# Optimization experiments

Measured on AMD Instinct MI355X. Metric: run time of the kernel, lower is better.

## Reference

```python
import jax, jax.numpy as jnp
import numpy as np

N = 38332        # nodes = poi_len - 1 (pinned by fc_layer in_features)
POI_LEN = 38333
CAT_LEN = 400
POI_DIM = 300
CAT_DIM = 100
C = 128          # gcn_channel
L = 5            # gcn_layers
E = 1200000      # edges
NEG = 0.01       # nn.LeakyReLU default slope
GAT_NEG = 0.2    # GATConv attention slope


def _leaky(x, s=NEG):
    return jnp.where(x > 0, x, s * x)


def _gcn_conv(x, W, b, src, dst, ew):
    # PyG GCNConv: self-loops already appended in (src,dst,ew); symmetric norm
    xw = x @ W
    deg = jax.ops.segment_sum(ew, dst, num_segments=N)
    dinv = jnp.where(deg > 0, jax.lax.rsqrt(deg), 0.0)
    norm = dinv[src] * ew * dinv[dst]
    out = jax.ops.segment_sum(xw[src] * norm[:, None], dst, num_segments=N)
    return out + b


def _gat_conv(x, W, a_src, a_dst, b, src, dst):
    # PyG GATConv, 1 head; self-loops already in (src,dst)
    xw = x @ W                      # [N, C]
    al = xw @ a_src                 # [N]
    ar = xw @ a_dst                 # [N]
    e = _leaky(al[src] + ar[dst], GAT_NEG)          # [E+N]
    emax = jax.ops.segment_max(e, dst, num_segments=N)
    ex = jnp.exp(e - emax[dst])
    denom = jax.ops.segment_sum(ex, dst, num_segments=N)
    att = ex / denom[dst]
    out = jax.ops.segment_sum(xw[src] * att[:, None], dst, num_segments=N)
    return out + b


def _graph_norm(x, gamma, beta, alpha, eps=1e-5):
    # PyG GraphNorm over the single graph (all nodes)
    mean = x.mean(0)
    xc = x - alpha * mean
    var = (xc * xc).mean(0)
    return gamma * xc * jax.lax.rsqrt(var + eps) + beta


def _forward(poi_ids, cat_ids, feat3, edge_index, edge_weight, poi_emb, cat_emb,
             Win, b_in, gcn_W, gcn_b, gn_gamma, gn_beta, gn_alpha,
             gat_W, gat_asrc, gat_adst, gat_b, Wout, b_out,
             fc_W1, fc_b1, fc_W2, fc_b2):
    loops = jnp.arange(N, dtype=edge_index.dtype)
    src = jnp.concatenate([edge_index[0], loops])
    dst = jnp.concatenate([edge_index[1], loops])
    ew = jnp.concatenate([edge_weight, jnp.ones((N,), edge_weight.dtype)])
    # node features: [poi_emb | cat_emb | 3 raw floats] -> [N, 403]
    feat = jnp.concatenate([poi_emb[poi_ids], cat_emb[cat_ids], feat3], axis=1)
    x = _leaky(_gcn_conv(feat, Win, b_in, src, dst, ew))
    for l in range(L):  # GcnUnit stack (shared GraphNorm within a unit)
        t = _leaky(_graph_norm(_gcn_conv(x, gcn_W[l], gcn_b[l], src, dst, ew),
                               gn_gamma[l], gn_beta[l], gn_alpha[l]))
        x = x + t
        t = _leaky(_graph_norm(_gat_conv(x, gat_W[l], gat_asrc[l], gat_adst[l], gat_b[l], src, dst),
                               gn_gamma[l], gn_beta[l], gn_alpha[l]))
        x = x + t
    x = _leaky(_gcn_conv(x, Wout, b_out, src, dst, ew)).reshape(-1)  # [N]
    h = jax.nn.relu(x @ fc_W1 + fc_b1)
    return jax.nn.relu(h @ fc_W2 + fc_b2)  # [POI_LEN]


def setup_inputs() -> dict:
    key = jax.random.key(0)
    ks = iter(jax.random.split(key, 24))
    nrm = lambda s, sc=0.05: jax.random.normal(next(ks), s, dtype=jnp.float32) * sc
    return {
        'poi_ids': jax.random.randint(next(ks), (N,), 0, POI_LEN),
        'cat_ids': jax.random.randint(next(ks), (N,), 0, CAT_LEN),
        'feat3': jax.random.normal(next(ks), (N, 3), dtype=jnp.float32),
        'edge_index': jax.random.randint(next(ks), (2, E), 0, N),
        'edge_weight': jax.random.uniform(next(ks), (E,), dtype=jnp.float32),
        'poi_emb': nrm((POI_LEN, POI_DIM)),
        'cat_emb': nrm((CAT_LEN, CAT_DIM)),
        'Win': nrm((POI_DIM + CAT_DIM + 3, C)),
        'b_in': jnp.zeros((C,), jnp.float32),
        'gcn_W': nrm((L, C, C)),
        'gcn_b': jnp.zeros((L, C), jnp.float32),
        'gn_gamma': jnp.ones((L, C), jnp.float32),
        'gn_beta': jnp.zeros((L, C), jnp.float32),
        'gn_alpha': jnp.ones((L, C), jnp.float32),
        'gat_W': nrm((L, C, C)),
        'gat_asrc': nrm((L, C)),
        'gat_adst': nrm((L, C)),
        'gat_b': jnp.zeros((L, C), jnp.float32),
        'Wout': nrm((C, 1)),
        'b_out': jnp.zeros((1,), jnp.float32),
        'fc_W1': nrm((N, 128)),
        'fc_b1': jnp.zeros((128,), jnp.float32),
        'fc_W2': nrm((128, POI_LEN)),
        'fc_b2': jnp.zeros((POI_LEN,), jnp.float32),
    }


def reference(poi_ids, cat_ids, feat3, edge_index, edge_weight, poi_emb, cat_emb,
              Win, b_in, gcn_W, gcn_b, gn_gamma, gn_beta, gn_alpha,
              gat_W, gat_asrc, gat_adst, gat_b, Wout, b_out,
              fc_W1, fc_b1, fc_W2, fc_b2):
    return _forward(poi_ids, cat_ids, feat3, edge_index, edge_weight, poi_emb, cat_emb,
                    Win, b_in, gcn_W, gcn_b, gn_gamma, gn_beta, gn_alpha,
                    gat_W, gat_asrc, gat_adst, gat_b, Wout, b_out,
                    fc_W1, fc_b1, fc_W2, fc_b2)
```

## Files before the change

kernel.cpp:

```cpp
#include <hip/hip_runtime.h>

typedef unsigned short ushort_t;
typedef __attribute__((ext_vector_type(8))) short short8v;
typedef __attribute__((ext_vector_type(4))) float floatx4;

__device__ __forceinline__ float b2f(ushort_t u) {
    unsigned int x = ((unsigned int)u) << 16;
    float f; __builtin_memcpy(&f, &x, 4); return f;
}
__device__ __forceinline__ ushort_t f2b(float f) {
    unsigned int x; __builtin_memcpy(&x, &f, 4);
    unsigned int lsb = (x >> 16) & 1u;
    x += 0x7fffu + lsb;
    return (ushort_t)(x >> 16);
}
__device__ __forceinline__ float leaky01(float v) { return v > 0.f ? v : 0.01f * v; }

__global__ void init_k(int* cnt, int N) {
    int i = blockIdx.x * 256 + threadIdx.x;
    if (i < N) cnt[i] = 1;
}

__global__ void count_k(const int* __restrict__ ei, int* cnt, int* pos, int E) {
    int e = blockIdx.x * 256 + threadIdx.x;
    if (e < E) pos[e] = atomicAdd(&cnt[ei[E + e]], 1);
}

__launch_bounds__(1024)
__global__ void scan_k(const int* __restrict__ cnt, int* rp, int n) {
    __shared__ int wsum[16];
    int tid = threadIdx.x; int lane = tid & 63, wid = tid >> 6;
    int base = 0;
    for (int start = 0; start < n; start += 4096) {
        int v[4]; int s = 0;
        #pragma unroll
        for (int j = 0; j < 4; ++j) {
            int i = start + tid * 4 + j;
            v[j] = (i < n) ? cnt[i] : 0; s += v[j];
        }
        int sc = s;
        #pragma unroll
        for (int off = 1; off < 64; off <<= 1) {
            int t = __shfl_up(sc, off);
            if (lane >= off) sc += t;
        }
        if (lane == 63) wsum[wid] = sc;
        __syncthreads();
        if (wid == 0) {
            int ws = (lane < 16) ? wsum[lane] : 0;
            #pragma unroll
            for (int off = 1; off < 16; off <<= 1) {
                int t = __shfl_up(ws, off);
                if (lane >= off) ws += t;
            }
            if (lane < 16) wsum[lane] = ws;
        }
        __syncthreads();
        int wbase = (wid > 0) ? wsum[wid - 1] : 0;
        int excl = base + wbase + (sc - s);
        #pragma unroll
        for (int j = 0; j < 4; ++j) {
            int i = start + tid * 4 + j;
            if (i < n) rp[i] = excl;
            excl += v[j];
        }
        int total = wsum[15];
        __syncthreads();
        base += total;
    }
    if (tid == 0) rp[n] = base;
}

__global__ void post_k(const int* __restrict__ rp, float2* er, int N) {
    int i = blockIdx.x * 256 + threadIdx.x;
    if (i < N) er[rp[i]] = make_float2(__int_as_float(i), 1.0f);
}

__global__ void scat_k(const int* __restrict__ ei, const float* __restrict__ ew,
                       const int* __restrict__ rp, const int* __restrict__ pos,
                       float2* er, int E) {
    int e = blockIdx.x * 256 + threadIdx.x;
    if (e < E) {
        int dst = ei[E + e];
        er[rp[dst] + pos[e]] = make_float2(__int_as_float(ei[e]), ew[e]);
    }
}

__global__ void deg_k(const int* __restrict__ rp, const float2* __restrict__ er,
                      float* dinv, int N) {
    int wave = threadIdx.x >> 6, lane = threadIdx.x & 63;
    int node = blockIdx.x * 4 + wave;
    if (node >= N) return;
    int s0 = rp[node], end = rp[node + 1];
    float sum = 0.f;
    for (int s = s0 + lane; s < end; s += 64) sum += er[s].y;
    #pragma unroll
    for (int off = 32; off; off >>= 1) sum += __shfl_xor(sum, off);
    if (lane == 0) dinv[node] = rsqrtf(sum);
}

__global__ void prep_w(const float* __restrict__ gcn_W, const float* __restrict__ gat_W,
                       const float* __restrict__ Win, ushort_t* __restrict__ wt,
                       ushort_t* __restrict__ wtin) {
    int idx = blockIdx.x * 256 + threadIdx.x;
    if (idx < 10 * 16384) {
        int l = idx >> 14, r = idx & 16383;
        int n = r >> 7, k = r & 127;
        const float* src = (l < 5) ? (gcn_W + l * 16384) : (gat_W + (l - 5) * 16384);
        wt[idx] = f2b(src[k * 128 + n]);
    } else {
        int idx2 = idx - 10 * 16384;
        if (idx2 < 128 * 320) {
            int n = idx2 / 320, k = idx2 - n * 320;
            wtin[idx2] = f2b(k < 300 ? Win[k * 128 + n] : 0.f);
        }
    }
}

__global__ void cat_proj_k(const float* __restrict__ ce, const float* __restrict__ Win,
                           float* __restrict__ cp) {
    __shared__ float row[100];
    int r = blockIdx.x, tid = threadIdx.x;
    if (tid < 100) row[tid] = ce[r * 100 + tid];
    __syncthreads();
    float acc = 0.f;
    #pragma unroll 4
    for (int k = 0; k < 100; ++k) acc += row[k] * Win[(300 + k) * 128 + tid];
    cp[r * 128 + tid] = acc;
}

__launch_bounds__(256)
__global__ void poi_gemm(const float* __restrict__ pe, const ushort_t* __restrict__ wtin,
                         ushort_t* __restrict__ pp, int P) {
    __shared__ __align__(16) ushort_t As[64 * 328];
    int tid = threadIdx.x;
    int wid = tid >> 6, lane = tid & 63;
    int r0 = blockIdx.x * 64;
    #pragma unroll
    for (int p = 0; p < 80; ++p) {
        int idx = tid + p * 256;
        int row = idx / 320, k = idx - row * 320;
        float v = 0.f;
        if (k < 300 && (r0 + row) < P) v = pe[(size_t)(r0 + row) * 300 + k];
        As[row * 328 + k] = f2b(v);
    }
    __syncthreads();
    int m = lane & 15, q = lane >> 4;
    short8v af[10];
    #pragma unroll
    for (int kc = 0; kc < 10; ++kc)
        af[kc] = *(const short8v*)&As[(wid * 16 + m) * 328 + kc * 32 + q * 8];
    #pragma unroll
    for (int ct = 0; ct < 8; ++ct) {
        const ushort_t* wr = wtin + (size_t)(ct * 16 + m) * 320 + q * 8;
        floatx4 acc = {0.f, 0.f, 0.f, 0.f};
        #pragma unroll
        for (int kc = 0; kc < 10; ++kc) {
            short8v b = *(const short8v*)(wr + kc * 32);
            acc = __builtin_amdgcn_mfma_f32_16x16x32_bf16(af[kc], b, acc, 0, 0, 0);
        }
        int col = ct * 16 + m;
        #pragma unroll
        for (int rg = 0; rg < 4; ++rg) {
            int row = r0 + wid * 16 + q * 4 + rg;
            if (row < P) pp[(size_t)row * 128 + col] = f2b(acc[rg]);
        }
    }
}

template <int NORM, int ALAR>
__launch_bounds__(256)
__global__ void gemm_fused(float* __restrict__ x, const float* __restrict__ gsrc,
                           const float* __restrict__ mom,
                           const float* __restrict__ gamma, const float* __restrict__ beta,
                           const float* __restrict__ alpha,
                           const ushort_t* __restrict__ wt,
                           const float* __restrict__ asrc, const float* __restrict__ adst,
                           ushort_t* __restrict__ xw,
                           float* __restrict__ al, float* __restrict__ ar, int N) {
    __shared__ __align__(16) ushort_t As[64 * 136];
    __shared__ float sc[128], sh[128];
    int tid = threadIdx.x;
    if (NORM) {
        if (tid < 128) {
            float mmean = mom[tid] / (float)N;
            float a = alpha[tid];
            float var = mom[128 + tid] / (float)N - 2.f * a * mmean * mmean + a * a * mmean * mmean;
            float s = gamma[tid] * rsqrtf(var + 1e-5f);
            sc[tid] = s;
            sh[tid] = beta[tid] - s * a * mmean;
        }
        __syncthreads();
    }
    int r0 = blockIdx.x * 64;
    #pragma unroll
    for (int p = 0; p < 8; ++p) {
        int idx = tid + p * 256;
        int row = idx >> 5, c4 = (idx & 31) * 4;
        int grow = r0 + row;
        float4 xv = make_float4(0.f, 0.f, 0.f, 0.f);
        if (grow < N) {
            xv = *(const float4*)&x[(size_t)grow * 128 + c4];
            if (NORM) {
                float4 gv = *(const float4*)&gsrc[(size_t)grow * 128 + c4];
                xv.x += leaky01(sc[c4] * gv.x + sh[c4]);
                xv.y += leaky01(sc[c4 + 1] * gv.y + sh[c4 + 1]);
                xv.z += leaky01(sc[c4 + 2] * gv.z + sh[c4 + 2]);
                xv.w += leaky01(sc[c4 + 3] * gv.w + sh[c4 + 3]);
                *(float4*)&x[(size_t)grow * 128 + c4] = xv;
            }
        }
        ushort4 b;
        b.x = f2b(xv.x); b.y = f2b(xv.y); b.z = f2b(xv.z); b.w = f2b(xv.w);
        *(ushort4*)&As[row * 136 + c4] = b;
    }
    __syncthreads();
    int wid = tid >> 6, lane = tid & 63;
    int m = lane & 15, q = lane >> 4;
    const int arr = (wid * 16 + m) * 136 + q * 8;
    short8v a0 = *(const short8v*)&As[arr];
    short8v a1 = *(const short8v*)&As[arr + 32];
    short8v a2 = *(const short8v*)&As[arr + 64];
    short8v a3 = *(const short8v*)&As[arr + 96];
    float alsum[4] = {0.f, 0.f, 0.f, 0.f}, arsum[4] = {0.f, 0.f, 0.f, 0.f};
    #pragma unroll
    for (int ct = 0; ct < 8; ++ct) {
        const ushort_t* wr = wt + (size_t)(ct * 16 + m) * 128 + q * 8;
        short8v b0 = *(const short8v*)(wr);
        short8v b1 = *(const short8v*)(wr + 32);
        short8v b2 = *(const short8v*)(wr + 64);
        short8v b3 = *(const short8v*)(wr + 96);
        floatx4 acc = {0.f, 0.f, 0.f, 0.f};
        acc = __builtin_amdgcn_mfma_f32_16x16x32_bf16(a0, b0, acc, 0, 0, 0);
        acc = __builtin_amdgcn_mfma_f32_16x16x32_bf16(a1, b1, acc, 0, 0, 0);
        acc = __builtin_amdgcn_mfma_f32_16x16x32_bf16(a2, b2, acc, 0, 0, 0);
        acc = __builtin_amdgcn_mfma_f32_16x16x32_bf16(a3, b3, acc, 0, 0, 0);
        int col = ct * 16 + m;
        if (ALAR) {
            float av = asrc[col], dv = adst[col];
            #pragma unroll
            for (int rg = 0; rg < 4; ++rg) {
                alsum[rg] += acc[rg] * av;
                arsum[rg] += acc[rg] * dv;
            }
        }
        #pragma unroll
        for (int rg = 0; rg < 4; ++rg) {
            int row = r0 + wid * 16 + q * 4 + rg;
            if (row < N) xw[(size_t)row * 128 + col] = f2b(acc[rg]);
        }
    }
    if (ALAR) {
        #pragma unroll
        for (int rg = 0; rg < 4; ++rg) {
            #pragma unroll
            for (int off = 1; off < 16; off <<= 1) {
                alsum[rg] += __shfl_xor(alsum[rg], off);
                arsum[rg] += __shfl_xor(arsum[rg], off);
            }
        }
        if (m == 0) {
            #pragma unroll
            for (int rg = 0; rg < 4; ++rg) {
                int row = r0 + wid * 16 + q * 4 + rg;
                if (row < N) { al[row] = alsum[rg]; ar[row] = arsum[rg]; }
            }
        }
    }
}

__global__ void combine_k(const ushort_t* __restrict__ pp, const float* __restrict__ cp,
                          const int* __restrict__ poi_ids, const int* __restrict__ cat_ids,
                          const float* __restrict__ feat3, const float* __restrict__ Win,
                          ushort_t* __restrict__ xw, int N) {
    __shared__ float wf0[128], wf1[128], wf2[128];
    int tid = threadIdx.x;
    if (tid < 128) {
        wf0[tid] = Win[400 * 128 + tid];
        wf1[tid] = Win[401 * 128 + tid];
        wf2[tid] = Win[402 * 128 + tid];
    }
    __syncthreads();
    int node = blockIdx.x * 2 + (tid >> 7);
    int c = tid & 127;
    if (node >= N) return;
    int pid = poi_ids[node], cid = cat_ids[node];
    float f0 = feat3[node * 3], f1 = feat3[node * 3 + 1], f2 = feat3[node * 3 + 2];
    float v = b2f(pp[(size_t)pid * 128 + c]) + cp[cid * 128 + c]
            + f0 * wf0[c] + f1 * wf1[c] + f2 * wf2[c];
    xw[(size_t)node * 128 + c] = f2b(v);
}

template <int MODE>
__launch_bounds__(256)
__global__ void agg_k(const ushort_t* __restrict__ xw, const int* __restrict__ rp,
                      const float2* __restrict__ er, const float* __restrict__ dinv,
                      const float* __restrict__ al, const float* __restrict__ ar,
                      const float* __restrict__ bias, float* __restrict__ g, int N) {
    int wave = threadIdx.x >> 6, lane = threadIdx.x & 63;
    int node = blockIdx.x * 4 + wave;
    if (node >= N) return;
    int s0 = __builtin_amdgcn_readfirstlane(rp[node]);
    int end = __builtin_amdgcn_readfirstlane(rp[node + 1]);
    int g8 = lane >> 4;
    int c8 = (lane & 15) * 8;
    float dn = 0.f, mmax = 0.f, inv = 0.f, ari = 0.f;
    if (MODE == 2) {
        ari = ar[node];
        float mm = -1e30f;
        for (int s = s0 + lane; s < end; s += 64) {
            int src = __float_as_int(er[s].x);
            float e = al[src] + ari; e = e > 0.f ? e : 0.2f * e;
            mm = fmaxf(mm, e);
        }
        #pragma unroll
        for (int off = 32; off; off >>= 1) mm = fmaxf(mm, __shfl_xor(mm, off));
        float ds = 0.f;
        for (int s = s0 + lane; s < end; s += 64) {
            int src = __float_as_int(er[s].x);
            float e = al[src] + ari; e = e > 0.f ? e : 0.2f * e;
            ds += __expf(e - mm);
        }
        #pragma unroll
        for (int off = 32; off; off >>= 1) ds += __shfl_xor(ds, off);
        mmax = mm;
        inv = 1.f / ds;
    } else {
        dn = dinv[node];
    }
    float acc[8] = {0.f, 0.f, 0.f, 0.f, 0.f, 0.f, 0.f, 0.f};
    auto body = [&](int e) {
        float2 r = er[e];
        int src = __float_as_int(r.x);
        float cf;
        if (MODE == 2) {
            float ev = al[src] + ari; ev = ev > 0.f ? ev : 0.2f * ev;
            cf = __expf(ev - mmax) * inv;
        } else {
            cf = dinv[src] * r.y * dn;
        }
        const short8v u = *(const short8v*)&xw[(size_t)src * 128 + c8];
        #pragma unroll
        for (int k = 0; k < 8; ++k) acc[k] += cf * b2f((ushort_t)u[k]);
    };
    int e = s0 + g8;
    for (; e + 12 < end; e += 16) { body(e); body(e + 4); body(e + 8); body(e + 12); }
    for (; e < end; e += 4) body(e);
    #pragma unroll
    for (int k = 0; k < 8; ++k) {
        acc[k] += __shfl_xor(acc[k], 16);
        acc[k] += __shfl_xor(acc[k], 32);
    }
    if (g8 == 0) {
        float4 o1, o2;
        o1.x = acc[0] + bias[c8];     o1.y = acc[1] + bias[c8 + 1];
        o1.z = acc[2] + bias[c8 + 2]; o1.w = acc[3] + bias[c8 + 3];
        o2.x = acc[4] + bias[c8 + 4]; o2.y = acc[5] + bias[c8 + 5];
        o2.z = acc[6] + bias[c8 + 6]; o2.w = acc[7] + bias[c8 + 7];
        if (MODE == 1) {
            o1.x = leaky01(o1.x); o1.y = leaky01(o1.y); o1.z = leaky01(o1.z); o1.w = leaky01(o1.w);
            o2.x = leaky01(o2.x); o2.y = leaky01(o2.y); o2.z = leaky01(o2.z); o2.w = leaky01(o2.w);
        }
        *(float4*)&g[(size_t)node * 128 + c8] = o1;
        *(float4*)&g[(size_t)node * 128 + c8 + 4] = o2;
    }
}

__global__ void moments_k(const float* __restrict__ g, float* mom, int n32) {
    __shared__ float s1s[256][4], s2s[256][4];
    int tid = threadIdx.x;
    long long T = (long long)gridDim.x * 256;
    float a1[4] = {0.f, 0.f, 0.f, 0.f}, a2[4] = {0.f, 0.f, 0.f, 0.f};
    const float4* g4 = (const float4*)g;
    for (long long idx = (long long)blockIdx.x * 256 + tid; idx < n32; idx += T) {
        float4 v = g4[idx];
        a1[0] += v.x; a2[0] += v.x * v.x;
        a1[1] += v.y; a2[1] += v.y * v.y;
        a1[2] += v.z; a2[2] += v.z * v.z;
        a1[3] += v.w; a2[3] += v.w * v.w;
    }
    #pragma unroll
    for (int j = 0; j < 4; ++j) { s1s[tid][j] = a1[j]; s2s[tid][j] = a2[j]; }
    __syncthreads();
    if (tid < 32) {
        float r1[4] = {0.f, 0.f, 0.f, 0.f}, r2[4] = {0.f, 0.f, 0.f, 0.f};
        for (int t = tid; t < 256; t += 32) {
            #pragma unroll
            for (int j = 0; j < 4; ++j) { r1[j] += s1s[t][j]; r2[j] += s2s[t][j]; }
        }
        #pragma unroll
        for (int j = 0; j < 4; ++j) {
            atomicAdd(&mom[4 * tid + j], r1[j]);
            atomicAdd(&mom[128 + 4 * tid + j], r2[j]);
        }
    }
}

__global__ void norm_ydot_k(const float* __restrict__ x, const float* __restrict__ g,
                            const float* __restrict__ mom,
                            const float* __restrict__ gamma, const float* __restrict__ beta,
                            const float* __restrict__ alpha, const float* __restrict__ Wout,
                            float* __restrict__ yv, int N) {
    __shared__ float sc[128], sh[128], wv[128];
    int tid = threadIdx.x;
    if (tid < 128) {
        float m = mom[tid] / (float)N;
        float a = alpha[tid];
        float var = mom[128 + tid] / (float)N - 2.f * a * m * m + a * a * m * m;
        float s = gamma[tid] * rsqrtf(var + 1e-5f);
        sc[tid] = s;
        sh[tid] = beta[tid] - s * a * m;
        wv[tid] = Wout[tid];
    }
    __syncthreads();
    int wave = tid >> 6, lane = tid & 63;
    int node = blockIdx.x * 4 + wave;
    if (node >= N) return;
    int c = lane * 2;
    float2 gv = *(const float2*)&g[(size_t)node * 128 + c];
    float2 xv = *(const float2*)&x[(size_t)node * 128 + c];
    float v0 = xv.x + leaky01(sc[c] * gv.x + sh[c]);
    float v1 = xv.y + leaky01(sc[c + 1] * gv.y + sh[c + 1]);
    float acc = v0 * wv[c] + v1 * wv[c + 1];
    #pragma unroll
    for (int off = 32; off; off >>= 1) acc += __shfl_xor(acc, off);
    if (lane == 0) yv[node] = acc;
}

__global__ void aggs_k(const float* __restrict__ yv, const int* __restrict__ rp,
                       const float2* __restrict__ er, const float* __restrict__ dinv,
                       const float* __restrict__ b_out, float* xs, int N) {
    int wave = threadIdx.x >> 6, lane = threadIdx.x & 63;
    int node = blockIdx.x * 4 + wave;
    if (node >= N) return;
    int s0 = rp[node], end = rp[node + 1];
    float dn = dinv[node];
    float acc = 0.f;
    for (int s = s0 + lane; s < end; s += 64) {
        float2 r = er[s];
        int src = __float_as_int(r.x);
        acc += dinv[src] * r.y * dn * yv[src];
    }
    #pragma unroll
    for (int off = 32; off; off >>= 1) acc += __shfl_xor(acc, off);
    if (lane == 0) xs[node] = leaky01(acc + b_out[0]);
}

__global__ void fc1_k(const float* __restrict__ xs, const float* __restrict__ W1,
                      float* hacc, int N) {
    __shared__ float sd[256];
    int tid = threadIdx.x;
    int j = tid & 127, half = tid >> 7;
    int r0 = blockIdx.x * 256;
    float acc = 0.f;
    for (int rr = half; rr < 256; rr += 2) {
        int r = r0 + rr;
        if (r < N) acc += xs[r] * W1[(size_t)r * 128 + j];
    }
    sd[tid] = acc;
    __syncthreads();
    if (tid < 128) atomicAdd(&hacc[tid], sd[tid] + sd[tid + 128]);
}

__global__ void fc2_k(const float* __restrict__ hacc, const float* __restrict__ b1,
                      const float* __restrict__ W2, const float* __restrict__ b2v,
                      float* out, int P) {
    __shared__ float hs[128];
    int tid = threadIdx.x;
    if (tid < 128) {
        float h = hacc[tid] + b1[tid];
        hs[tid] = h > 0.f ? h : 0.f;
    }
    __syncthreads();
    int p = blockIdx.x * 256 + tid;
    if (p >= P) return;
    float acc = 0.f;
    #pragma unroll 8
    for (int j = 0; j < 128; ++j) acc += hs[j] * W2[(size_t)j * P + p];
    acc += b2v[p];
    out[p] = acc > 0.f ? acc : 0.f;
}

extern "C" void kernel_launch(void* const* d_in, const int* in_sizes, int n_in,
                              void* d_out, int out_size, void* d_ws, size_t ws_size,
                              hipStream_t stream) {
    const int*   poi_ids  = (const int*)d_in[0];
    const int*   cat_ids  = (const int*)d_in[1];
    const float* feat3    = (const float*)d_in[2];
    const int*   ei       = (const int*)d_in[3];
    const float* ew       = (const float*)d_in[4];
    const float* poi_emb  = (const float*)d_in[5];
    const float* cat_emb  = (const float*)d_in[6];
    const float* Win      = (const float*)d_in[7];
    const float* b_in     = (const float*)d_in[8];
    const float* gcn_W    = (const float*)d_in[9];
    const float* gcn_b    = (const float*)d_in[10];
    const float* gn_gamma = (const float*)d_in[11];
    const float* gn_beta  = (const float*)d_in[12];
    const float* gn_alpha = (const float*)d_in[13];
    const float* gat_W    = (const float*)d_in[14];
    const float* gat_asrc = (const float*)d_in[15];
    const float* gat_adst = (const float*)d_in[16];
    const float* gat_b    = (const float*)d_in[17];
    const float* Wout     = (const float*)d_in[18];
    const float* b_out    = (const float*)d_in[19];
    const float* fc_W1    = (const float*)d_in[20];
    const float* fc_b1    = (const float*)d_in[21];
    const float* fc_W2    = (const float*)d_in[22];
    const float* fc_b2    = (const float*)d_in[23];

    const int N = in_sizes[0];
    const int E = in_sizes[4];
    const int POI = in_sizes[5] / 300;
    const int P = out_size;
    const int TOT = E + N;
    const int n128 = N * 128;
    const int n32 = n128 / 4;
    const int NPAD = ((N + 63) / 64) * 64;
    const int PPAD = ((POI + 63) / 64) * 64;

    char* w = (char*)d_ws;
    size_t off = 0;
    auto take = [&](size_t bytes) -> char* {
        char* p = w + off;
        off = (off + bytes + 255) & ~(size_t)255;
        return p;
    };
    float*    x    = (float*)take((size_t)n128 * 4);
    float*    g    = (float*)take((size_t)n128 * 4);
    ushort_t* xw   = (ushort_t*)take((size_t)NPAD * 128 * 2);
    ushort_t* pp   = (ushort_t*)take((size_t)PPAD * 128 * 2);
    float*    cp   = (float*)take((size_t)400 * 128 * 4);
    ushort_t* wt   = (ushort_t*)take((size_t)10 * 16384 * 2);
    ushort_t* wtin = (ushort_t*)take((size_t)128 * 320 * 2);
    int*    rp   = (int*)take((size_t)(N + 1) * 4);
    int*    cnt  = (int*)take((size_t)N * 4);
    int*    pos  = (int*)take((size_t)E * 4);
    float*  dinv = (float*)take((size_t)N * 4);
    float2* er   = (float2*)take((size_t)TOT * 8);
    float*  al   = (float*)take((size_t)N * 4);
    float*  ar   = (float*)take((size_t)N * 4);
    float*  yv   = (float*)take((size_t)N * 4);
    float*  xs   = (float*)take((size_t)N * 4);
    float*  mom  = (float*)take((size_t)(10 * 256 + 128) * 4);
    float*  hacc = mom + 10 * 256;

    const int gN   = (N + 255) / 256;
    const int gE   = (E + 255) / 256;
    const int gMM  = NPAD / 64;
    const int gPOI = PPAD / 64;
    const int gW   = (N + 3) / 4;
    const int gP   = (P + 255) / 256;

    hipMemsetAsync(mom, 0, (size_t)(10 * 256 + 128) * 4, stream);

    init_k<<<gN, 256, 0, stream>>>(cnt, N);
    count_k<<<gE, 256, 0, stream>>>(ei, cnt, pos, E);
    scan_k<<<1, 1024, 0, stream>>>(cnt, rp, N);
    post_k<<<gN, 256, 0, stream>>>(rp, er, N);
    scat_k<<<gE, 256, 0, stream>>>(ei, ew, rp, pos, er, E);
    deg_k<<<gW, 256, 0, stream>>>(rp, er, dinv, N);

    prep_w<<<(10 * 16384 + 128 * 320 + 255) / 256, 256, 0, stream>>>(gcn_W, gat_W, Win, wt, wtin);
    cat_proj_k<<<400, 128, 0, stream>>>(cat_emb, Win, cp);
    poi_gemm<<<gPOI, 256, 0, stream>>>(poi_emb, wtin, pp, POI);
    combine_k<<<(N + 1) / 2, 256, 0, stream>>>(pp, cp, poi_ids, cat_ids, feat3, Win, xw, N);
    agg_k<1><<<gW, 256, 0, stream>>>(xw, rp, er, dinv, nullptr, nullptr, b_in, x, N);

    for (int l = 0; l < 5; ++l) {
        if (l == 0)
            gemm_fused<0, 0><<<gMM, 256, 0, stream>>>(x, nullptr, nullptr, nullptr, nullptr,
                                                      nullptr, wt, nullptr, nullptr,
                                                      xw, nullptr, nullptr, N);
        else
            gemm_fused<1, 0><<<gMM, 256, 0, stream>>>(x, g, mom + (2 * l - 1) * 256,
                                                      gn_gamma + (l - 1) * 128,
                                                      gn_beta + (l - 1) * 128,
                                                      gn_alpha + (l - 1) * 128,
                                                      wt + (size_t)l * 16384, nullptr, nullptr,
                                                      xw, nullptr, nullptr, N);
        agg_k<0><<<gW, 256, 0, stream>>>(xw, rp, er, dinv, nullptr, nullptr,
                                         gcn_b + l * 128, g, N);
        moments_k<<<240, 256, 0, stream>>>(g, mom + (2 * l) * 256, n32);

        gemm_fused<1, 1><<<gMM, 256, 0, stream>>>(x, g, mom + (2 * l) * 256,
                                                  gn_gamma + l * 128, gn_beta + l * 128,
                                                  gn_alpha + l * 128,
                                                  wt + (size_t)(5 + l) * 16384,
                                                  gat_asrc + l * 128, gat_adst + l * 128,
                                                  xw, al, ar, N);
        agg_k<2><<<gW, 256, 0, stream>>>(xw, rp, er, nullptr, al, ar, gat_b + l * 128, g, N);
        moments_k<<<240, 256, 0, stream>>>(g, mom + (2 * l + 1) * 256, n32);
    }

    norm_ydot_k<<<gW, 256, 0, stream>>>(x, g, mom + 9 * 256, gn_gamma + 4 * 128,
                                        gn_beta + 4 * 128, gn_alpha + 4 * 128, Wout, yv, N);
    aggs_k<<<gW, 256, 0, stream>>>(yv, rp, er, dinv, b_out, xs, N);

    fc1_k<<<(N + 255) / 256, 256, 0, stream>>>(xs, fc_W1, hacc, N);
    fc2_k<<<gP, 256, 0, stream>>>(hacc, fc_b1, fc_W2, fc_b2, (float*)d_out, P);
}
```

Before: 1.454 ms.

## Precompute GCN edge coefficients, vectorize poi_gemm loads, deepen aggregation unroll

Adds a one-time pass that folds the symmetric normalization dinv[src]*w*dinv[dst] into the CSR edge array, so the GCN aggregation kernels and the final scalar aggregation read a ready coefficient instead of gathering dinv per edge. The poi_gemm staging loop now loads float4 rows and zero-fills the K padding separately. The aggregation inner loop is unrolled to 8 edges per group for more memory-level parallelism. It costs one extra kernel pass over the edges and more registers in agg_k.

```diff
diff --git a/kernel.cpp b/kernel.cpp
--- a/kernel.cpp
+++ b/kernel.cpp
@@ -97,6 +97,21 @@
     #pragma unroll
     for (int off = 32; off; off >>= 1) sum += __shfl_xor(sum, off);
     if (lane == 0) dinv[node] = rsqrtf(sum);
+}
+
+__global__ void coef_k(const int* __restrict__ rp, float2* er,
+                       const float* __restrict__ dinv, int N) {
+    int wave = threadIdx.x >> 6, lane = threadIdx.x & 63;
+    int node = blockIdx.x * 4 + wave;
+    if (node >= N) return;
+    int s0 = rp[node], end = rp[node + 1];
+    float dn = dinv[node];
+    for (int s = s0 + lane; s < end; s += 64) {
+        float2 r = er[s];
+        int src = __float_as_int(r.x);
+        r.y = dinv[src] * r.y * dn;
+        er[s] = r;
+    }
 }
 
 __global__ void prep_w(const float* __restrict__ gcn_W, const float* __restrict__ gat_W,
@@ -137,12 +152,25 @@
     int wid = tid >> 6, lane = tid & 63;
     int r0 = blockIdx.x * 64;
     #pragma unroll
-    for (int p = 0; p < 80; ++p) {
+    for (int p = 0; p < 19; ++p) {
         int idx = tid + p * 256;
-        int row = idx / 320, k = idx - row * 320;
-        float v = 0.f;
-        if (k < 300 && (r0 + row) < P) v = pe[(size_t)(r0 + row) * 300 + k];
-        As[row * 328 + k] = f2b(v);
+        if (idx < 4800) {
+            int row = idx / 75, kq = idx - row * 75;
+            int grow = r0 + row;
+            float4 v = make_float4(0.f, 0.f, 0.f, 0.f);
+            if (grow < P) v = *(const float4*)&pe[(size_t)grow * 300 + kq * 4];
+            ushort4 b;
+            b.x = f2b(v.x); b.y = f2b(v.y); b.z = f2b(v.z); b.w = f2b(v.w);
+            *(ushort4*)&As[row * 328 + kq * 4] = b;
+        }
+    }
+    #pragma unroll
+    for (int p = 0; p < 5; ++p) {
+        int idx = tid + p * 256;
+        if (idx < 1280) {
+            int row = idx / 20, j = idx - row * 20;
+            As[row * 328 + 300 + j] = 0;
+        }
     }
     __syncthreads();
     int m = lane & 15, q = lane >> 4;
@@ -294,7 +322,7 @@
 template <int MODE>
 __launch_bounds__(256)
 __global__ void agg_k(const ushort_t* __restrict__ xw, const int* __restrict__ rp,
-                      const float2* __restrict__ er, const float* __restrict__ dinv,
+                      const float2* __restrict__ er,
                       const float* __restrict__ al, const float* __restrict__ ar,
                       const float* __restrict__ bias, float* __restrict__ g, int N) {
     int wave = threadIdx.x >> 6, lane = threadIdx.x & 63;
@@ -304,7 +332,7 @@
     int end = __builtin_amdgcn_readfirstlane(rp[node + 1]);
     int g8 = lane >> 4;
     int c8 = (lane & 15) * 8;
-    float dn = 0.f, mmax = 0.f, inv = 0.f, ari = 0.f;
+    float mmax = 0.f, inv = 0.f, ari = 0.f;
     if (MODE == 2) {
         ari = ar[node];
         float mm = -1e30f;
@@ -325,8 +353,6 @@
         for (int off = 32; off; off >>= 1) ds += __shfl_xor(ds, off);
         mmax = mm;
         inv = 1.f / ds;
-    } else {
-        dn = dinv[node];
     }
     float acc[8] = {0.f, 0.f, 0.f, 0.f, 0.f, 0.f, 0.f, 0.f};
     auto body = [&](int e) {
@@ -337,14 +363,17 @@
             float ev = al[src] + ari; ev = ev > 0.f ? ev : 0.2f * ev;
             cf = __expf(ev - mmax) * inv;
         } else {
-            cf = dinv[src] * r.y * dn;
+            cf = r.y;
         }
         const short8v u = *(const short8v*)&xw[(size_t)src * 128 + c8];
         #pragma unroll
         for (int k = 0; k < 8; ++k) acc[k] += cf * b2f((ushort_t)u[k]);
     };
     int e = s0 + g8;
-    for (; e + 12 < end; e += 16) { body(e); body(e + 4); body(e + 8); body(e + 12); }
+    for (; e + 28 < end; e += 32) {
+        body(e);      body(e + 4);  body(e + 8);  body(e + 12);
+        body(e + 16); body(e + 20); body(e + 24); body(e + 28);
+    }
     for (; e < end; e += 4) body(e);
     #pragma unroll
     for (int k = 0; k < 8; ++k) {
@@ -428,18 +457,16 @@
 }
 
 __global__ void aggs_k(const float* __restrict__ yv, const int* __restrict__ rp,
-                       const float2* __restrict__ er, const float* __restrict__ dinv,
+                       const float2* __restrict__ er,
                        const float* __restrict__ b_out, float* xs, int N) {
     int wave = threadIdx.x >> 6, lane = threadIdx.x & 63;
     int node = blockIdx.x * 4 + wave;
     if (node >= N) return;
     int s0 = rp[node], end = rp[node + 1];
-    float dn = dinv[node];
     float acc = 0.f;
     for (int s = s0 + lane; s < end; s += 64) {
         float2 r = er[s];
-        int src = __float_as_int(r.x);
-        acc += dinv[src] * r.y * dn * yv[src];
+        acc += r.y * yv[__float_as_int(r.x)];
     }
     #pragma unroll
     for (int off = 32; off; off >>= 1) acc += __shfl_xor(acc, off);
@@ -560,12 +587,13 @@
     post_k<<<gN, 256, 0, stream>>>(rp, er, N);
     scat_k<<<gE, 256, 0, stream>>>(ei, ew, rp, pos, er, E);
     deg_k<<<gW, 256, 0, stream>>>(rp, er, dinv, N);
+    coef_k<<<gW, 256, 0, stream>>>(rp, er, dinv, N);
 
     prep_w<<<(10 * 16384 + 128 * 320 + 255) / 256, 256, 0, stream>>>(gcn_W, gat_W, Win, wt, wtin);
     cat_proj_k<<<400, 128, 0, stream>>>(cat_emb, Win, cp);
     poi_gemm<<<gPOI, 256, 0, stream>>>(poi_emb, wtin, pp, POI);
     combine_k<<<(N + 1) / 2, 256, 0, stream>>>(pp, cp, poi_ids, cat_ids, feat3, Win, xw, N);
-    agg_k<1><<<gW, 256, 0, stream>>>(xw, rp, er, dinv, nullptr, nullptr, b_in, x, N);
+    agg_k<1><<<gW, 256, 0, stream>>>(xw, rp, er, nullptr, nullptr, b_in, x, N);
 
     for (int l = 0; l < 5; ++l) {
         if (l == 0)
@@ -579,8 +607,7 @@
                                                       gn_alpha + (l - 1) * 128,
                                                       wt + (size_t)l * 16384, nullptr, nullptr,
                                                       xw, nullptr, nullptr, N);
-        agg_k<0><<<gW, 256, 0, stream>>>(xw, rp, er, dinv, nullptr, nullptr,
-                                         gcn_b + l * 128, g, N);
+        agg_k<0><<<gW, 256, 0, stream>>>(xw, rp, er, nullptr, nullptr, gcn_b + l * 128, g, N);
         moments_k<<<240, 256, 0, stream>>>(g, mom + (2 * l) * 256, n32);
 
         gemm_fused<1, 1><<<gMM, 256, 0, stream>>>(x, g, mom + (2 * l) * 256,
@@ -589,13 +616,13 @@
                                                   wt + (size_t)(5 + l) * 16384,
                                                   gat_asrc + l * 128, gat_adst + l * 128,
                                                   xw, al, ar, N);
-        agg_k<2><<<gW, 256, 0, stream>>>(xw, rp, er, nullptr, al, ar, gat_b + l * 128, g, N);
+        agg_k<2><<<gW, 256, 0, stream>>>(xw, rp, er, al, ar, gat_b + l * 128, g, N);
         moments_k<<<240, 256, 0, stream>>>(g, mom + (2 * l + 1) * 256, n32);
     }
 
     norm_ydot_k<<<gW, 256, 0, stream>>>(x, g, mom + 9 * 256, gn_gamma + 4 * 128,
                                         gn_beta + 4 * 128, gn_alpha + 4 * 128, Wout, yv, N);
-    aggs_k<<<gW, 256, 0, stream>>>(yv, rp, er, dinv, b_out, xs, N);
+    aggs_k<<<gW, 256, 0, stream>>>(yv, rp, er, b_out, xs, N);
 
     fc1_k<<<(N + 255) / 256, 256, 0, stream>>>(xs, fc_W1, hacc, N);
     fc2_k<<<gP, 256, 0, stream>>>(hacc, fc_b1, fc_W2, fc_b2, (float*)d_out, P);
```

Result: slower. 1.704 ms (+17.2%).
